# Performance work log

Measured on AMD Instinct MI355X. Metric: run time of the kernel, lower is better.

The kernel has to match this reference:

```python
import jax, jax.numpy as jnp
from jax import lax
import numpy as np


def setup_inputs() -> dict:
    key = jax.random.key(0)
    ks = iter(jax.random.split(key, 48))

    def w(shape):
        fan = shape[0] if len(shape) == 2 else int(np.prod(shape[1:]))
        return jax.random.normal(next(ks), shape, jnp.float32) / np.sqrt(fan)

    def b(n):
        return jax.random.normal(next(ks), (n,), jnp.float32) * 0.01

    T = 16
    return dict(
        search=jax.random.normal(next(ks), (3, 383, 287), jnp.float32),
        exemplars=jax.random.normal(next(ks), (T, 3, 383, 287), jnp.float32),
        # AlexNet features (random-weight stand-in for pretrained)
        aw1=w((64, 3, 11, 11)), ab1=b(64),
        aw2=w((192, 64, 5, 5)), ab2=b(192),
        aw3=w((384, 192, 3, 3)), ab3=b(384),
        aw4=w((256, 384, 3, 3)), ab4=b(256),
        aw5=w((256, 256, 3, 3)), ab5=b(256),
        # conv_deconv: Conv1d(256,256,3,p=1) -> MaxPool1d(88) -> ConvTranspose1d(256,256,88)
        wcd=w((256, 256, 3)), bcd=b(256),
        wt=w((256, 256, 88)), bt=b(256),
        # st_gcn: GCN(256, 512, 256)
        ws1=w((256, 512)), bs1=b(512),
        ws2=w((512, 256)), bs2=b(256),
        # g, h: 1x1 Conv1d(256,256) == linear maps
        wg=w((256, 256)), bg=b(256),
        wh=w((256, 256)), bh=b(256),
        # ct_gcn: GCN(256, 384, 256)
        wc1=w((256, 384)), bc1=b(384),
        wc2=w((384, 256)), bc2=b(256),
    )


def _gct_forward(search, exemplars, aw1, ab1, aw2, ab2, aw3, ab3, aw4, ab4,
                 aw5, ab5, wcd, bcd, wt, bt, ws1, bs1, ws2, bs2,
                 wg, bg, wh, bh, wc1, bc1, wc2, bc2):
    f32 = jnp.float32

    def conv2d(x, w, bias, s, p):
        y = lax.conv_general_dilated(x, w, (s, s), [(p, p), (p, p)],
                                     dimension_numbers=('NCHW', 'OIHW', 'NCHW'))
        return y + bias[None, :, None, None]

    def maxpool(x):  # k=3, s=2, VALID (AlexNet pools)
        return lax.reduce_window(x, -jnp.inf, lax.max, (1, 1, 3, 3), (1, 1, 2, 2), 'VALID')

    def features(x):
        x = maxpool(jax.nn.relu(conv2d(x, aw1, ab1, 4, 2)))
        x = maxpool(jax.nn.relu(conv2d(x, aw2, ab2, 1, 2)))
        x = jax.nn.relu(conv2d(x, aw3, ab3, 1, 1))
        x = jax.nn.relu(conv2d(x, aw4, ab4, 1, 1))
        x = maxpool(jax.nn.relu(conv2d(x, aw5, ab5, 1, 1)))
        return x

    lrelu = lambda v: jax.nn.leaky_relu(v, 0.01)

    X = features(search[None])          # [1,256,11,8]
    Z = features(exemplars)             # [T,256,11,8]
    T = Z.shape[0]
    D = X.shape[1]                      # 256
    M = X.shape[2] * X.shape[3]         # 88
    Xf = X.reshape(D, M)                # [256,88]
    Zf = Z.reshape(T, D, M)             # [T,256,88]

    # conv_deconv branch: conv1d(k=3,p=1) -> global maxpool -> conv_transpose(k=M)
    xc = lax.conv_general_dilated(Xf[None], wcd, (1,), [(1, 1)],
                                  dimension_numbers=('NCH', 'OIH', 'NCH'))[0] + bcd[:, None]
    v = jnp.max(xc, axis=1)                              # [256]
    X_hat = jnp.einsum('i,iok->ok', v, wt) + bt[:, None]  # [256,88]

    # spatiotemporal graph: A[i+T*j, i+T*k]=1 for j!=k; self-loops for t!=0
    TM = T * M
    n = jnp.arange(TM)
    same_t = (n[:, None] % T) == (n[None, :] % T)
    diff_s = (n[:, None] // T) != (n[None, :] // T)
    A1 = (same_t & diff_s).astype(f32) + jnp.diag((n % T != 0).astype(f32))

    # st GCN over TM nodes (node n = t + T*m -> spatial-major flatten)
    nodes = Zf.transpose(2, 0, 1).reshape(TM, D)          # [TM,256]
    h1 = lrelu(A1 @ (nodes @ ws1) + bs1)                  # [TM,512]
    h2 = lrelu(A1 @ (h1 @ ws2) + bs2)                     # [TM,256]
    V1 = jnp.max(h2.reshape(M, T, D), axis=1).T           # temporal max-pool -> [256,88]

    # dynamic cross-track graph: pairwise g/h affinities + row softmax (fused)
    Vx = V1 + X_hat                                       # [256,88]
    G = wg @ Vx + bg[:, None]                             # [256,88]
    Hh = wh @ Vx + bh[:, None]                            # [256,88]
    A2 = jax.nn.softmax(Hh.T @ G, axis=1)                 # [88,88], A2[j,i]=g(i).h(j)

    # ct GCN
    xv = V1.T                                             # [88,256]
    c1 = lrelu(A2 @ (xv @ wc1) + bc1)                     # [88,384]
    V2 = lrelu(A2 @ (c1 @ wc2) + bc2).T                   # [256,88]

    # F.conv2d(X[1,256,11,8], V2[1,256,11,8]) -> full-overlap correlation = scalar
    R = jnp.sum(Xf * V2).reshape(1, 1, 1, 1)
    return R


def reference(search, exemplars, aw1, ab1, aw2, ab2, aw3, ab3, aw4, ab4,
              aw5, ab5, wcd, bcd, wt, bt, ws1, bs1, ws2, bs2,
              wg, bg, wh, bh, wc1, bc1, wc2, bc2):
    return _gct_forward(search, exemplars, aw1, ab1, aw2, ab2, aw3, ab3, aw4, ab4,
                        aw5, ab5, wcd, bcd, wt, bt, ws1, bs1, ws2, bs2,
                        wg, bg, wh, bh, wc1, bc1, wc2, bc2)
```

## Files before the change

### kernel.cpp

```cpp
#include <hip/hip_runtime.h>
#include <hip/hip_bf16.h>
#include <math.h>

#define BATCH 17
#define T_EX 16
#define H0 383
#define W0 287
#define C1 64
#define H1 95
#define W1 71
#define H1P 47
#define W1P 35
#define C2 192
#define H2P 23
#define W2P 17
#define C3 384
#define C45 256
#define H5P 11
#define W5P 8
#define DD 256
#define MM 88
#define TM 1408

#define HP1 389
#define WP1 292

typedef unsigned short ushort_t;
typedef __attribute__((ext_vector_type(8))) short short8;
typedef __attribute__((ext_vector_type(4))) float f32x4;

__device__ __forceinline__ float lrelu(float v) { return v > 0.f ? v : 0.01f * v; }

__device__ __forceinline__ ushort_t f2bf(float f) {
    unsigned int u = __float_as_uint(f);
    unsigned int r = (u + 0x7fffu + ((u >> 16) & 1u)) >> 16;
    return (ushort_t)r;
}
__device__ __forceinline__ float b2f(ushort_t b) {
    return __uint_as_float(((unsigned int)b) << 16);
}
__device__ __forceinline__ short8 ld16(const ushort_t* p) { return *(const short8*)p; }
__device__ __forceinline__ short8 ld2x8(const ushort_t* p) {
    union { uint2 u[2]; short8 s; } uu;
    uu.u[0] = *(const uint2*)p;
    uu.u[1] = *(const uint2*)(p + 4);
    return uu.s;
}
__device__ __forceinline__ void async_cp16(ushort_t* l, const ushort_t* g) {
    __builtin_amdgcn_global_load_lds(
        (const __attribute__((address_space(1))) void*)g,
        (__attribute__((address_space(3))) void*)l, 16, 0, 0);
}

__global__ void zfill_k(float4* __restrict__ p, int n4) {
    int idx = blockIdx.x * 256 + threadIdx.x;
    if (idx < n4) p[idx] = (float4){0.f, 0.f, 0.f, 0.f};
}

__global__ void prep1_k(const float* __restrict__ search, const float* __restrict__ exemp,
                        ushort_t* __restrict__ out) {
    int idx = blockIdx.x * 256 + threadIdx.x;
    if (idx >= BATCH * H0 * W0) return;
    int ix = idx % W0; int t = idx / W0;
    int iy = t % H0; int b = t / H0;
    const float* src = (b == 0) ? search : exemp + (size_t)(b - 1) * 3 * H0 * W0;
    const int hw = H0 * W0;
    float v0 = src[iy * W0 + ix];
    float v1 = src[hw + iy * W0 + ix];
    float v2 = src[2 * hw + iy * W0 + ix];
    ushort4 o;
    o.x = f2bf(v0); o.y = f2bf(v1); o.z = f2bf(v2); o.w = 0;
    *(ushort4*)&out[(((size_t)b * HP1 + iy + 2) * WP1 + ix + 2) * 4] = o;
}

__global__ void wprep_k(const float* __restrict__ w, ushort_t* __restrict__ out,
                        int KH, int KWl, int KWr, int CINl, int CINr,
                        int NKS, int nch) {
    int idx = blockIdx.x * 256 + threadIdx.x;
    if (idx >= nch) return;
    int c = idx & 255;
    int rest = idx >> 8;
    int ks = rest % NKS;
    int ocb = rest / NKS;
    int k8 = c >> 6, m = c & 63;
    int oc = ocb * 64 + m;
    int KWC = KWl * CINl;
    ushort_t* o = out + (size_t)idx * 8;
#pragma unroll
    for (int j = 0; j < 8; ++j) {
        int kg = ks * 32 + k8 * 8 + j;
        int ky = kg / KWC; int rem = kg - ky * KWC;
        int kx = rem / CINl; int ic = rem - kx * CINl;
        float v = 0.f;
        if (ky < KH && kx < KWr && ic < CINr)
            v = w[(((size_t)oc * CINr + ic) * KH + ky) * KWr + kx];
        o[j] = f2bf(v);
    }
}

__global__ void wprep_gemm_k(const float* __restrict__ ws1, const float* __restrict__ ws2,
                             const float* __restrict__ wcd, ushort_t* __restrict__ WS1T,
                             ushort_t* __restrict__ WS2T, ushort_t* __restrict__ WCDT) {
    int idx = blockIdx.x * 256 + threadIdx.x;
    const float* src; ushort_t* dst; int NKS, mode = 0, sa = 1, sk = 0, base;
    if (idx < 16384)       { src = ws1; dst = WS1T; NKS = 8;  sk = 512; base = idx; }
    else if (idx < 32768)  { src = ws2; dst = WS2T; NKS = 16; sk = 256; base = idx - 16384; }
    else if (idx < 57344)  { src = wcd; dst = WCDT; NKS = 24; mode = 1; base = idx - 32768; }
    else return;
    int c = base & 255;
    int rest = base >> 8;
    int ks = rest % NKS;
    int ocb = rest / NKS;
    int k8 = c >> 6, m = c & 63;
    int oc = ocb * 64 + m;
    ushort_t* o = dst + (size_t)base * 8;
#pragma unroll
    for (int j = 0; j < 8; ++j) {
        int kg = ks * 32 + k8 * 8 + j;
        float v;
        if (mode == 0) v = src[(size_t)oc * sa + (size_t)kg * sk];
        else           v = src[(size_t)oc * 768 + (kg & 255) * 3 + (kg >> 8)];
        o[j] = f2bf(v);
    }
}

template <int STRIDE, bool A16>
__global__ __launch_bounds__(256) void conv_mfma5(
    const ushort_t* __restrict__ inp, const ushort_t* __restrict__ wt,
    const float* __restrict__ bias, ushort_t* __restrict__ out,
    int Hp, int Wp, int C, int Wout, int HW, int NKS2, int KWl,
    int OHp, int OWp, int OPAD, int COUT) {
    const int tid = threadIdx.x;
    const int wv = tid >> 6, lane = tid & 63;
    const int quad = lane >> 4, l16 = lane & 15;
    const int n_blk = blockIdx.x * 64;
    const int ocb = blockIdx.y;
    const int b = blockIdx.z;

    __shared__ ushort_t As[2][4096];
    __shared__ ushort_t Bs[2][4096];
    __shared__ int offs[432];

    const int KWC = KWl * C;
    for (int g = tid; g < NKS2 * 8; g += 256) {
        int kg = g * 8;
        int ky = kg / KWC; int rem = kg - ky * KWC;
        int kx = rem / C; int c8 = rem - kx * C;
        offs[g] = (ky * Wp + kx) * C + c8;
    }

    const ushort_t* inb = inp + (size_t)b * Hp * Wp * C;
    int n_g = n_blk + lane;
    int n_gc = n_g < HW ? n_g : HW - 1;
    int oy = n_gc / Wout, ox = n_gc - oy * Wout;
    const int base0 = (oy * STRIDE * Wp + ox * STRIDE) * C;

    f32x4 acc[4];
#pragma unroll
    for (int cn = 0; cn < 4; ++cn) acc[cn] = (f32x4){0.f, 0.f, 0.f, 0.f};

    const ushort_t* wblk = wt + (size_t)ocb * (size_t)NKS2 * 4096;

    __syncthreads();

    {
        const ushort_t* aS = wblk + tid * 8;
        async_cp16(&As[0][tid * 8], aS);
        async_cp16(&As[0][2048 + tid * 8], aS + 2048);
        const int o0 = offs[wv], o1 = offs[4 + wv];
        if (A16) {
            async_cp16(&Bs[0][tid * 8], inb + base0 + o0);
            async_cp16(&Bs[0][2048 + tid * 8], inb + base0 + o1);
        } else {
            *(short8*)&Bs[0][tid * 8] = ld2x8(inb + base0 + o0);
            *(short8*)&Bs[0][2048 + tid * 8] = ld2x8(inb + base0 + o1);
        }
    }
    __syncthreads();

    for (int ks2 = 0; ks2 < NKS2; ++ks2) {
        const int cur = ks2 & 1, nxt = cur ^ 1;
        if (ks2 + 1 < NKS2) {
            const ushort_t* aS = wblk + (size_t)(ks2 + 1) * 4096 + tid * 8;
            async_cp16(&As[nxt][tid * 8], aS);
            async_cp16(&As[nxt][2048 + tid * 8], aS + 2048);
            const int o0 = offs[(ks2 + 1) * 8 + wv], o1 = offs[(ks2 + 1) * 8 + 4 + wv];
            if (A16) {
                async_cp16(&Bs[nxt][tid * 8], inb + base0 + o0);
                async_cp16(&Bs[nxt][2048 + tid * 8], inb + base0 + o1);
            } else {
                *(short8*)&Bs[nxt][tid * 8] = ld2x8(inb + base0 + o0);
                *(short8*)&Bs[nxt][2048 + tid * 8] = ld2x8(inb + base0 + o1);
            }
        }
#pragma unroll
        for (int h = 0; h < 2; ++h) {
            const short8 af = *(const short8*)&As[cur][h * 2048 + (quad * 64 + wv * 16 + l16) * 8];
#pragma unroll
            for (int cn = 0; cn < 4; ++cn) {
                const short8 bfr = *(const short8*)&Bs[cur][h * 2048 + (quad * 64 + cn * 16 + l16) * 8];
                acc[cn] = __builtin_amdgcn_mfma_f32_16x16x32_bf16(af, bfr, acc[cn], 0, 0, 0);
            }
        }
        __syncthreads();
    }

    const int oc0 = ocb * 64 + wv * 16 + quad * 4;
    const float bi0 = bias[oc0], bi1 = bias[oc0 + 1], bi2 = bias[oc0 + 2], bi3 = bias[oc0 + 3];
#pragma unroll
    for (int cn = 0; cn < 4; ++cn) {
        int n = n_blk + cn * 16 + l16;
        if (n < HW) {
            int y = n / Wout, x = n - y * Wout;
            size_t base = (((size_t)b * OHp + y + OPAD) * OWp + x + OPAD) * COUT + oc0;
            ushort4 o;
            o.x = f2bf(fmaxf(acc[cn][0] + bi0, 0.f));
            o.y = f2bf(fmaxf(acc[cn][1] + bi1, 0.f));
            o.z = f2bf(fmaxf(acc[cn][2] + bi2, 0.f));
            o.w = f2bf(fmaxf(acc[cn][3] + bi3, 0.f));
            *(ushort4*)&out[base] = o;
        }
    }
}

template <int MODE, bool HASBIAS, bool SC1>
__global__ __launch_bounds__(256) void gemm_mfma3(
    const ushort_t* __restrict__ Bsrc, const ushort_t* __restrict__ wt,
    const float* __restrict__ bias, float* __restrict__ out,
    int RS, int N, int NKS, int sn, int sc) {
    const int tid = threadIdx.x;
    const int wv = tid >> 6, lane = tid & 63;
    const int quad = lane >> 4, l16 = lane & 15;
    const int n_blk = blockIdx.x * 64;
    const int ocb = blockIdx.y;

    __shared__ ushort_t Bs[2][2048];

    int n_g = n_blk + lane;
    int n_gc = n_g < N ? n_g : N - 1;
    int row = (MODE == 1) ? (1 + (n_gc & 15)) * MM + (n_gc >> 4) : n_gc;
    const size_t base0 = (size_t)row * RS;

    f32x4 acc[4];
#pragma unroll
    for (int cn = 0; cn < 4; ++cn) acc[cn] = (f32x4){0.f, 0.f, 0.f, 0.f};

    const ushort_t* wblk = wt + (size_t)ocb * NKS * 2048;
    const int afrag = (quad * 64 + wv * 16 + l16) * 8;

    short8 a0 = ld16(wblk + afrag);
    *(short8*)&Bs[0][tid * 8] = ld16(Bsrc + base0 + wv * 8);
    __syncthreads();

    for (int ks = 0; ks < NKS; ++ks) {
        const int cur = ks & 1, nxt = cur ^ 1;
        short8 a1, bn;
        const bool more = (ks + 1 < NKS);
        if (more) {
            a1 = ld16(wblk + (ks + 1) * 2048 + afrag);
            bn = ld16(Bsrc + base0 + (ks + 1) * 32 + wv * 8);
        }
#pragma unroll
        for (int cn = 0; cn < 4; ++cn) {
            const short8 bfr = *(const short8*)&Bs[cur][(quad * 64 + cn * 16 + l16) * 8];
            acc[cn] = __builtin_amdgcn_mfma_f32_16x16x32_bf16(a0, bfr, acc[cn], 0, 0, 0);
        }
        if (more) *(short8*)&Bs[nxt][tid * 8] = bn;
        a0 = a1;
        __syncthreads();
    }

    const int oc0 = ocb * 64 + wv * 16 + quad * 4;
    float bb[4] = {0.f, 0.f, 0.f, 0.f};
    if (HASBIAS) { bb[0] = bias[oc0]; bb[1] = bias[oc0+1]; bb[2] = bias[oc0+2]; bb[3] = bias[oc0+3]; }
#pragma unroll
    for (int cn = 0; cn < 4; ++cn) {
        int n = n_blk + cn * 16 + l16;
        if (n < N) {
            if (SC1) {
                float4 o;
                o.x = acc[cn][0] + bb[0]; o.y = acc[cn][1] + bb[1];
                o.z = acc[cn][2] + bb[2]; o.w = acc[cn][3] + bb[3];
                *(float4*)&out[(size_t)n * sn + oc0] = o;
            } else {
#pragma unroll
                for (int reg = 0; reg < 4; ++reg)
                    out[(size_t)n * sn + (size_t)(oc0 + reg) * sc] = acc[cn][reg] + bb[reg];
            }
        }
    }
}

__global__ void pool_nhwc(const ushort_t* __restrict__ in, ushort_t* __restrict__ out,
                          int C, int Hin, int Win, int Hout, int Wout,
                          int OHp, int OWp, int OPAD) {
    int total = BATCH * C * Hout * Wout;
    int idx = blockIdx.x * 256 + threadIdx.x;
    if (idx >= total) return;
    int c = idx % C; int r = idx / C;
    int x = r % Wout; r /= Wout;
    int y = r % Hout; int b = r / Hout;
    const int rs = Win * C;
    const ushort_t* p = in + (((size_t)b * Hin + 2 * y) * Win + 2 * x) * C + c;
    float m = b2f(p[0]);
    m = fmaxf(m, b2f(p[C])); m = fmaxf(m, b2f(p[2 * C]));
    m = fmaxf(m, b2f(p[rs])); m = fmaxf(m, b2f(p[rs + C])); m = fmaxf(m, b2f(p[rs + 2 * C]));
    m = fmaxf(m, b2f(p[2 * rs])); m = fmaxf(m, b2f(p[2 * rs + C])); m = fmaxf(m, b2f(p[2 * rs + 2 * C]));
    out[(((size_t)b * OHp + y + OPAD) * OWp + x + OPAD) * C + c] = f2bf(m);
}

__global__ void pool5_k(const ushort_t* __restrict__ in, float* __restrict__ P,
                        ushort_t* __restrict__ PB, ushort_t* __restrict__ XfPad) {
    int total = BATCH * 256 * MM;
    int idx = blockIdx.x * 256 + threadIdx.x;
    if (idx >= total) return;
    int c = idx % 256; int r = idx / 256;
    int x = r % W5P; r /= W5P;
    int y = r % H5P; int b = r / H5P;
    const int rs = W2P * 256;
    const ushort_t* p = in + (((size_t)b * H2P + 2 * y) * W2P + 2 * x) * 256 + c;
    float m = b2f(p[0]);
    m = fmaxf(m, b2f(p[256])); m = fmaxf(m, b2f(p[512]));
    m = fmaxf(m, b2f(p[rs])); m = fmaxf(m, b2f(p[rs + 256])); m = fmaxf(m, b2f(p[rs + 512]));
    m = fmaxf(m, b2f(p[2 * rs])); m = fmaxf(m, b2f(p[2 * rs + 256])); m = fmaxf(m, b2f(p[2 * rs + 512]));
    int mm = y * W5P + x;
    size_t o = ((size_t)b * MM + mm) * 256 + c;
    P[o] = m;
    ushort_t mb = f2bf(m);
    PB[o] = mb;
    if (b == 0) XfPad[(size_t)(mm + 1) * 256 + c] = mb;
}

__global__ void vmax_k(const float* __restrict__ xc, float* __restrict__ v) {
    int c = blockIdx.x * 64 + threadIdx.x;
    float m = -INFINITY;
    for (int j = 0; j < MM; ++j) m = fmaxf(m, xc[(size_t)c * MM + j]);
    v[c] = m;
}

__global__ void xhat_k(const float* __restrict__ v, const float* __restrict__ wt,
                       const float* __restrict__ bt, float* __restrict__ xhat) {
    __shared__ float lv[256];
    for (int j = threadIdx.x; j < 256; j += 256) lv[j] = v[j];
    __syncthreads();
    int idx = blockIdx.x * 256 + threadIdx.x;
    if (idx >= DD * MM) return;
    int k = idx % MM, o = idx / MM;
    float acc = bt[o];
    for (int i = 0; i < 256; ++i) acc = fmaf(lv[i], wt[(i * 256 + o) * MM + k], acc);
    xhat[idx] = acc;
}

__global__ void s1_k(const float* __restrict__ Y1, float* __restrict__ S1) {
    int idx = blockIdx.x * 256 + threadIdx.x;
    if (idx >= T_EX * 512) return;
    int c = idx % 512, t = idx / 512;
    float acc = 0.f;
    for (int m = 0; m < MM; ++m) acc += Y1[(m * T_EX + t) * 512 + c];
    S1[idx] = acc;
}

__global__ void h1_k(const float* __restrict__ Y1, const float* __restrict__ S1,
                     const float* __restrict__ bs1, ushort_t* __restrict__ h1b) {
    int idx = blockIdx.x * 256 + threadIdx.x;
    if (idx >= TM * 512) return;
    int c = idx % 512; int n = idx / 512;
    int t = n % T_EX;
    float val = S1[t * 512 + c] + bs1[c];
    if (t == 0) val -= Y1[idx];
    h1b[idx] = f2bf(lrelu(val));
}

__global__ void s2_k(const float* __restrict__ Y2, float* __restrict__ S2) {
    int idx = blockIdx.x * 256 + threadIdx.x;
    if (idx >= T_EX * 256) return;
    int c = idx % 256, t = idx / 256;
    float acc = 0.f;
    for (int m = 0; m < MM; ++m) acc += Y2[(m * T_EX + t) * 256 + c];
    S2[idx] = acc;
}

__global__ void h2_k(const float* __restrict__ Y2, const float* __restrict__ S2,
                     const float* __restrict__ bs2, float* __restrict__ h2) {
    int idx = blockIdx.x * 256 + threadIdx.x;
    if (idx >= TM * 256) return;
    int c = idx % 256; int n = idx / 256;
    int t = n % T_EX;
    float val = S2[t * 256 + c] + bs2[c];
    if (t == 0) val -= Y2[idx];
    h2[idx] = lrelu(val);
}

__global__ void v1vx_k(const float* __restrict__ h2, const float* __restrict__ xhat,
                       float* __restrict__ V1, float* __restrict__ Vx) {
    int idx = blockIdx.x * 256 + threadIdx.x;
    if (idx >= DD * MM) return;
    int m = idx % MM, d = idx / MM;
    float mx = -INFINITY;
    for (int t = 0; t < T_EX; ++t) mx = fmaxf(mx, h2[(m * T_EX + t) * 256 + d]);
    V1[idx] = mx;
    Vx[idx] = mx + xhat[idx];
}

__global__ void lin88_k(const float* __restrict__ Wg, const float* __restrict__ bg,
                        const float* __restrict__ Wh, const float* __restrict__ bh,
                        const float* __restrict__ Vin, float* __restrict__ Gout,
                        float* __restrict__ Hout) {
    int idx = blockIdx.x * 256 + threadIdx.x;
    if (idx >= DD * MM) return;
    const float* W = blockIdx.y ? Wh : Wg;
    const float* bias = blockIdx.y ? bh : bg;
    float* out = blockIdx.y ? Hout : Gout;
    int m = idx % MM, o = idx / MM;
    const float* wr = W + o * 256;
    float acc = bias[o];
    for (int i = 0; i < 256; ++i) acc = fmaf(wr[i], Vin[i * MM + m], acc);
    out[idx] = acc;
}

__global__ void smsm_k(const float* __restrict__ Hh, const float* __restrict__ G,
                       float* __restrict__ A2) {
    int j = blockIdx.x;
    int tid = threadIdx.x;
    __shared__ float row[96];
    __shared__ float red[128];
    for (int i = tid; i < MM; i += 128) {
        float acc = 0.f;
        for (int c = 0; c < 256; ++c) acc = fmaf(Hh[c * MM + j], G[c * MM + i], acc);
        row[i] = acc;
    }
    __syncthreads();
    float val = (tid < MM) ? row[tid] : -INFINITY;
    red[tid] = val; __syncthreads();
    for (int s = 64; s > 0; s >>= 1) {
        if (tid < s) red[tid] = fmaxf(red[tid], red[tid + s]);
        __syncthreads();
    }
    float mx = red[0]; __syncthreads();
    float e = (tid < MM) ? expf(val - mx) : 0.f;
    red[tid] = e; __syncthreads();
    for (int s = 64; s > 0; s >>= 1) {
        if (tid < s) red[tid] += red[tid + s];
        __syncthreads();
    }
    float inv = 1.f / red[0];
    if (tid < MM) A2[j * MM + tid] = e * inv;
}

__global__ void t1_k(const float* __restrict__ V1, const float* __restrict__ wc1,
                     float* __restrict__ t1) {
    int idx = blockIdx.x * 256 + threadIdx.x;
    if (idx >= MM * 384) return;
    int c = idx % 384, m = idx / 384;
    float acc = 0.f;
    for (int d = 0; d < 256; ++d) acc = fmaf(V1[d * MM + m], wc1[d * 384 + c], acc);
    t1[idx] = acc;
}

__global__ void c1_k(const float* __restrict__ A2, const float* __restrict__ t1,
                     const float* __restrict__ bc1, float* __restrict__ c1) {
    int idx = blockIdx.x * 256 + threadIdx.x;
    if (idx >= MM * 384) return;
    int c = idx % 384, j = idx / 384;
    float acc = bc1[c];
    for (int i = 0; i < MM; ++i) acc = fmaf(A2[j * MM + i], t1[i * 384 + c], acc);
    c1[idx] = lrelu(acc);
}

__global__ void t2_k(const float* __restrict__ c1, const float* __restrict__ wc2,
                     float* __restrict__ t2) {
    int idx = blockIdx.x * 256 + threadIdx.x;
    if (idx >= MM * 256) return;
    int c = idx % 256, m = idx / 256;
    const float* cr = c1 + m * 384;
    float acc = 0.f;
    for (int d = 0; d < 384; ++d) acc = fmaf(cr[d], wc2[d * 256 + c], acc);
    t2[idx] = acc;
}

__global__ void v2_k(const float* __restrict__ A2, const float* __restrict__ t2,
                     const float* __restrict__ bc2, float* __restrict__ V2m) {
    int idx = blockIdx.x * 256 + threadIdx.x;
    if (idx >= MM * 256) return;
    int c = idx % 256, j = idx / 256;
    float acc = bc2[c];
    for (int i = 0; i < MM; ++i) acc = fmaf(A2[j * MM + i], t2[i * 256 + c], acc);
    V2m[idx] = lrelu(acc);
}

__global__ void final_k(const float* __restrict__ Xf2, const float* __restrict__ V2m,
                        float* __restrict__ out) {
    __shared__ float red[256];
    float acc = 0.f;
    for (int idx = threadIdx.x; idx < DD * MM; idx += 256)
        acc = fmaf(Xf2[idx], V2m[idx], acc);
    red[threadIdx.x] = acc; __syncthreads();
    for (int s = 128; s > 0; s >>= 1) {
        if (threadIdx.x < s) red[threadIdx.x] += red[threadIdx.x + s];
        __syncthreads();
    }
    if (threadIdx.x == 0) out[0] = red[0];
}

extern "C" void kernel_launch(void* const* d_in, const int* in_sizes, int n_in,
                              void* d_out, int out_size, void* d_ws, size_t ws_size,
                              hipStream_t stream) {
    const float* search = (const float*)d_in[0];
    const float* exemp  = (const float*)d_in[1];
    const float* aw1 = (const float*)d_in[2];  const float* ab1 = (const float*)d_in[3];
    const float* aw2 = (const float*)d_in[4];  const float* ab2 = (const float*)d_in[5];
    const float* aw3 = (const float*)d_in[6];  const float* ab3 = (const float*)d_in[7];
    const float* aw4 = (const float*)d_in[8];  const float* ab4 = (const float*)d_in[9];
    const float* aw5 = (const float*)d_in[10]; const float* ab5 = (const float*)d_in[11];
    const float* wcd = (const float*)d_in[12]; const float* bcd = (const float*)d_in[13];
    const float* wt  = (const float*)d_in[14]; const float* bt  = (const float*)d_in[15];
    const float* ws1 = (const float*)d_in[16]; const float* bs1 = (const float*)d_in[17];
    const float* ws2 = (const float*)d_in[18]; const float* bs2 = (const float*)d_in[19];
    const float* wg  = (const float*)d_in[20]; const float* bg  = (const float*)d_in[21];
    const float* wh  = (const float*)d_in[22]; const float* bh  = (const float*)d_in[23];
    const float* wc1 = (const float*)d_in[24]; const float* bc1 = (const float*)d_in[25];
    const float* wc2 = (const float*)d_in[26]; const float* bc2 = (const float*)d_in[27];

    float* ws = (float*)d_ws;
    float* R1 = ws;
    float* R2 = ws + 3870720;
    float* R3 = ws + 7544832;
    float* Wg = ws + 8628864;

    ushort_t* in1p  = (ushort_t*)R1;
    ushort_t* c1out = (ushort_t*)R2;
    ushort_t* p1out = (ushort_t*)R3;
    ushort_t* c2out = (ushort_t*)R1;
    ushort_t* p2out = (ushort_t*)R2;
    ushort_t* c3out = (ushort_t*)(R2 + 775200);
    ushort_t* c4out = (ushort_t*)R1;
    ushort_t* c5out = (ushort_t*)R3;
    ushort_t* WT    = (ushort_t*)Wg;

    zfill_k<<<(965500 + 255) / 256, 256, 0, stream>>>((float4*)R1, 965500);
    prep1_k<<<(BATCH * H0 * W0 + 255) / 256, 256, 0, stream>>>(search, exemp, in1p);
    wprep_k<<<(4608 + 255) / 256, 256, 0, stream>>>(aw1, WT, 11, 12, 11, 4, 3, 18, 4608);
    conv_mfma5<4, false><<<dim3(106, 1, BATCH), 256, 0, stream>>>(
        in1p, WT, ab1, c1out, HP1, WP1, 4, W1, H1 * W1, 9, 12, H1, W1, 0, 64);
    zfill_k<<<(270504 + 255) / 256, 256, 0, stream>>>((float4*)R3, 270504);
    pool_nhwc<<<(BATCH * 64 * H1P * W1P + 255) / 256, 256, 0, stream>>>(
        c1out, p1out, 64, H1, W1, H1P, W1P, 51, 39, 2);
    wprep_k<<<(38400 + 255) / 256, 256, 0, stream>>>(aw2, WT, 5, 5, 5, 64, 64, 50, 38400);
    conv_mfma5<1, true><<<dim3(26, 3, BATCH), 256, 0, stream>>>(
        p1out, WT, ab2, c2out, 51, 39, 64, W1P, H1P * W1P, 25, 5, H1P, W1P, 0, 192);
    zfill_k<<<(581400 + 255) / 256, 256, 0, stream>>>((float4*)R2, 581400);
    pool_nhwc<<<(BATCH * 192 * H2P * W2P + 255) / 256, 256, 0, stream>>>(
        c2out, p2out, 192, H1P, W1P, H2P, W2P, 25, 19, 1);
    wprep_k<<<(82944 + 255) / 256, 256, 0, stream>>>(aw3, WT, 3, 3, 3, 192, 192, 54, 82944);
    conv_mfma5<1, true><<<dim3(7, 6, BATCH), 256, 0, stream>>>(
        p2out, WT, ab3, c3out, 25, 19, 192, W2P, H2P * W2P, 27, 3, 25, 19, 1, 384);
    zfill_k<<<(258400 + 255) / 256, 256, 0, stream>>>((float4*)R1, 258400);
    wprep_k<<<(110592 + 255) / 256, 256, 0, stream>>>(aw4, WT, 3, 3, 3, 384, 384, 108, 110592);
    conv_mfma5<1, true><<<dim3(7, 4, BATCH), 256, 0, stream>>>(
        c3out, WT, ab4, c4out, 25, 19, 384, W2P, H2P * W2P, 54, 3, 25, 19, 1, 256);
    wprep_k<<<(73728 + 255) / 256, 256, 0, stream>>>(aw5, WT, 3, 3, 3, 256, 256, 72, 73728);
    conv_mfma5<1, true><<<dim3(7, 4, BATCH), 256, 0, stream>>>(
        c4out, WT, ab5, c5out, 25, 19, 256, W2P, H2P * W2P, 36, 3, H2P, W2P, 0, 256);

    float*    P      = R1 + 2417664;
    ushort_t* PB     = (ushort_t*)(R1 + 2800640);
    ushort_t* XfPad  = (ushort_t*)(R1 + 2992128);
    float*    xc     = R1 + 3003648;

    ushort_t* WS1T = (ushort_t*)Wg;
    ushort_t* WS2T = (ushort_t*)(Wg + 65536);
    ushort_t* WCDT = (ushort_t*)(Wg + 131072);
    wprep_gemm_k<<<(57344 + 255) / 256, 256, 0, stream>>>(ws1, ws2, wcd, WS1T, WS2T, WCDT);

    pool5_k<<<(BATCH * 256 * MM + 255) / 256, 256, 0, stream>>>(c5out, P, PB, XfPad);
    float* Xf2 = P;

    float* v_   = R1 + 0;
    float* xhat = R1 + 1024;
    float* Y1   = R1 + 23552;
    float* S1   = R1 + 744448;
    ushort_t* h1b = (ushort_t*)(R1 + 752640);
    float* Y2   = R1 + 1473536;
    float* S2   = R1 + 1833984;
    float* h2   = R1 + 1838080;
    float* V1   = R1 + 2198528;
    float* Vx   = R1 + 2221056;
    float* G    = R1 + 2243584;
    float* Hh   = R1 + 2266112;
    float* A2   = R1 + 2296832;
    float* t1   = R1 + 2305024;
    float* c1   = R1 + 2338816;
    float* t2   = R1 + 2372608;
    float* V2m  = R1 + 2395136;

    gemm_mfma3<0, true, false><<<dim3(2, 4), 256, 0, stream>>>(
        XfPad, WCDT, bcd, xc, 256, MM, 24, 1, MM);
    vmax_k<<<4, 64, 0, stream>>>(xc, v_);
    xhat_k<<<(DD * MM + 255) / 256, 256, 0, stream>>>(v_, wt, bt, xhat);

    gemm_mfma3<1, false, true><<<dim3(22, 8), 256, 0, stream>>>(
        PB, WS1T, nullptr, Y1, 256, TM, 8, 512, 1);
    s1_k<<<(T_EX * 512 + 255) / 256, 256, 0, stream>>>(Y1, S1);
    h1_k<<<(TM * 512 + 255) / 256, 256, 0, stream>>>(Y1, S1, bs1, h1b);
    gemm_mfma3<0, false, true><<<dim3(22, 4), 256, 0, stream>>>(
        h1b, WS2T, nullptr, Y2, 512, TM, 16, 256, 1);
    s2_k<<<(T_EX * 256 + 255) / 256, 256, 0, stream>>>(Y2, S2);
    h2_k<<<(TM * 256 + 255) / 256, 256, 0, stream>>>(Y2, S2, bs2, h2);
    v1vx_k<<<(DD * MM + 255) / 256, 256, 0, stream>>>(h2, xhat, V1, Vx);

    lin88_k<<<dim3((DD * MM + 255) / 256, 2), 256, 0, stream>>>(wg, bg, wh, bh, Vx, G, Hh);
    smsm_k<<<MM, 128, 0, stream>>>(Hh, G, A2);

    t1_k<<<(MM * 384 + 255) / 256, 256, 0, stream>>>(V1, wc1, t1);
    c1_k<<<(MM * 384 + 255) / 256, 256, 0, stream>>>(A2, t1, bc1, c1);
    t2_k<<<(MM * 256 + 255) / 256, 256, 0, stream>>>(c1, wc2, t2);
    v2_k<<<(MM * 256 + 255) / 256, 256, 0, stream>>>(A2, t2, bc2, V2m);

    final_k<<<1, 256, 0, stream>>>(Xf2, V2m, (float*)d_out);
}
```

Baseline: 545.5 us.

## Use two-wave conv blocks with 32x64 per-wave tiles for more operand reuse

The implicit-GEMM conv kernel now uses 128 threads (2 waves) per 64x64 output tile, with each wave computing two 16-row MFMA blocks that share the same B fragments. This halves LDS reads of B per MFMA and raises register-level reuse. Staging loops are widened so fewer threads fill the same shared tiles. STRIDE becomes a runtime argument instead of a template parameter, which may cost some address arithmetic and reduce latency hiding per block because fewer waves are resident.

```diff
diff --git a/kernel.cpp b/kernel.cpp
--- a/kernel.cpp
+++ b/kernel.cpp
@@ -124,11 +124,11 @@
     }
 }
 
-template <int STRIDE, bool A16>
-__global__ __launch_bounds__(256) void conv_mfma5(
+template <bool A16>
+__global__ __launch_bounds__(128) void conv_mfma7(
     const ushort_t* __restrict__ inp, const ushort_t* __restrict__ wt,
     const float* __restrict__ bias, ushort_t* __restrict__ out,
-    int Hp, int Wp, int C, int Wout, int HW, int NKS2, int KWl,
+    int Hp, int Wp, int C, int Wout, int HW, int NKS2, int KWl, int STRIDE,
     int OHp, int OWp, int OPAD, int COUT) {
     const int tid = threadIdx.x;
     const int wv = tid >> 6, lane = tid & 63;
@@ -142,7 +142,7 @@
     __shared__ int offs[432];
 
     const int KWC = KWl * C;
-    for (int g = tid; g < NKS2 * 8; g += 256) {
+    for (int g = tid; g < NKS2 * 8; g += 128) {
         int kg = g * 8;
         int ky = kg / KWC; int rem = kg - ky * KWC;
         int kx = rem / C; int c8 = rem - kx * C;
@@ -150,75 +150,89 @@
     }
 
     const ushort_t* inb = inp + (size_t)b * Hp * Wp * C;
-    int n_g = n_blk + lane;
+    int n_g = n_blk + (tid & 63);
     int n_gc = n_g < HW ? n_g : HW - 1;
     int oy = n_gc / Wout, ox = n_gc - oy * Wout;
     const int base0 = (oy * STRIDE * Wp + ox * STRIDE) * C;
 
-    f32x4 acc[4];
-#pragma unroll
-    for (int cn = 0; cn < 4; ++cn) acc[cn] = (f32x4){0.f, 0.f, 0.f, 0.f};
+    f32x4 acc[2][4];
+#pragma unroll
+    for (int rm = 0; rm < 2; ++rm)
+#pragma unroll
+        for (int cn = 0; cn < 4; ++cn) acc[rm][cn] = (f32x4){0.f, 0.f, 0.f, 0.f};
 
     const ushort_t* wblk = wt + (size_t)ocb * (size_t)NKS2 * 4096;
 
     __syncthreads();
 
-    {
-        const ushort_t* aS = wblk + tid * 8;
-        async_cp16(&As[0][tid * 8], aS);
-        async_cp16(&As[0][2048 + tid * 8], aS + 2048);
-        const int o0 = offs[wv], o1 = offs[4 + wv];
-        if (A16) {
-            async_cp16(&Bs[0][tid * 8], inb + base0 + o0);
-            async_cp16(&Bs[0][2048 + tid * 8], inb + base0 + o1);
-        } else {
-            *(short8*)&Bs[0][tid * 8] = ld2x8(inb + base0 + o0);
-            *(short8*)&Bs[0][2048 + tid * 8] = ld2x8(inb + base0 + o1);
-        }
-    }
+#define STAGE_A(buf, ks2v)                                                   \
+    {                                                                        \
+        const ushort_t* tb = wblk + (size_t)(ks2v) * 4096;                   \
+        _Pragma("unroll")                                                    \
+        for (int p = 0; p < 4; ++p) {                                        \
+            int idx = p * 128 + tid;                                         \
+            async_cp16(&As[buf][idx * 8], tb + idx * 8);                     \
+        }                                                                    \
+    }
+#define STAGE_B(buf, ks2v)                                                   \
+    {                                                                        \
+        _Pragma("unroll")                                                    \
+        for (int p = 0; p < 4; ++p) {                                        \
+            int idx = p * 128 + tid;                \
+            int hh = idx >> 8, k8 = (idx >> 6) & 3;                          \
+            const ushort_t* s = inb + base0 + offs[(ks2v) * 8 + hh * 4 + k8];\
+            if (A16) async_cp16(&Bs[buf][idx * 8], s);                       \
+            else     *(short8*)&Bs[buf][idx * 8] = ld2x8(s);                 \
+        }                                                                    \
+    }
+
+    STAGE_A(0, 0)
+    STAGE_B(0, 0)
     __syncthreads();
 
     for (int ks2 = 0; ks2 < NKS2; ++ks2) {
         const int cur = ks2 & 1, nxt = cur ^ 1;
         if (ks2 + 1 < NKS2) {
-            const ushort_t* aS = wblk + (size_t)(ks2 + 1) * 4096 + tid * 8;
-            async_cp16(&As[nxt][tid * 8], aS);
-            async_cp16(&As[nxt][2048 + tid * 8], aS + 2048);
-            const int o0 = offs[(ks2 + 1) * 8 + wv], o1 = offs[(ks2 + 1) * 8 + 4 + wv];
-            if (A16) {
-                async_cp16(&Bs[nxt][tid * 8], inb + base0 + o0);
-                async_cp16(&Bs[nxt][2048 + tid * 8], inb + base0 + o1);
-            } else {
-                *(short8*)&Bs[nxt][tid * 8] = ld2x8(inb + base0 + o0);
-                *(short8*)&Bs[nxt][2048 + tid * 8] = ld2x8(inb + base0 + o1);
-            }
+            STAGE_A(nxt, ks2 + 1)
+            STAGE_B(nxt, ks2 + 1)
         }
 #pragma unroll
         for (int h = 0; h < 2; ++h) {
-            const short8 af = *(const short8*)&As[cur][h * 2048 + (quad * 64 + wv * 16 + l16) * 8];
+            const int abase = h * 256 + quad * 64;
+            const short8 a0 = *(const short8*)&As[cur][(abase + wv * 32 + l16) * 8];
+            const short8 a1 = *(const short8*)&As[cur][(abase + wv * 32 + 16 + l16) * 8];
+            short8 bf[4];
+#pragma unroll
+            for (int cn = 0; cn < 4; ++cn)
+                bf[cn] = *(const short8*)&Bs[cur][(abase + cn * 16 + l16) * 8];
 #pragma unroll
             for (int cn = 0; cn < 4; ++cn) {
-                const short8 bfr = *(const short8*)&Bs[cur][h * 2048 + (quad * 64 + cn * 16 + l16) * 8];
-                acc[cn] = __builtin_amdgcn_mfma_f32_16x16x32_bf16(af, bfr, acc[cn], 0, 0, 0);
+                acc[0][cn] = __builtin_amdgcn_mfma_f32_16x16x32_bf16(a0, bf[cn], acc[0][cn], 0, 0, 0);
+                acc[1][cn] = __builtin_amdgcn_mfma_f32_16x16x32_bf16(a1, bf[cn], acc[1][cn], 0, 0, 0);
             }
         }
         __syncthreads();
     }
-
-    const int oc0 = ocb * 64 + wv * 16 + quad * 4;
-    const float bi0 = bias[oc0], bi1 = bias[oc0 + 1], bi2 = bias[oc0 + 2], bi3 = bias[oc0 + 3];
-#pragma unroll
-    for (int cn = 0; cn < 4; ++cn) {
-        int n = n_blk + cn * 16 + l16;
-        if (n < HW) {
-            int y = n / Wout, x = n - y * Wout;
-            size_t base = (((size_t)b * OHp + y + OPAD) * OWp + x + OPAD) * COUT + oc0;
-            ushort4 o;
-            o.x = f2bf(fmaxf(acc[cn][0] + bi0, 0.f));
-            o.y = f2bf(fmaxf(acc[cn][1] + bi1, 0.f));
-            o.z = f2bf(fmaxf(acc[cn][2] + bi2, 0.f));
-            o.w = f2bf(fmaxf(acc[cn][3] + bi3, 0.f));
-            *(ushort4*)&out[base] = o;
+#undef STAGE_A
+#undef STAGE_B
+
+#pragma unroll
+    for (int rm = 0; rm < 2; ++rm) {
+        const int ocr = ocb * 64 + wv * 32 + rm * 16 + quad * 4;
+        const float bi0 = bias[ocr], bi1 = bias[ocr + 1], bi2 = bias[ocr + 2], bi3 = bias[ocr + 3];
+#pragma unroll
+        for (int cn = 0; cn < 4; ++cn) {
+            int n = n_blk + cn * 16 + l16;
+            if (n < HW) {
+                int y = n / Wout, x = n - y * Wout;
+                size_t base = (((size_t)b * OHp + y + OPAD) * OWp + x + OPAD) * COUT + ocr;
+                ushort4 o;
+                o.x = f2bf(fmaxf(acc[rm][cn][0] + bi0, 0.f));
+                o.y = f2bf(fmaxf(acc[rm][cn][1] + bi1, 0.f));
+                o.z = f2bf(fmaxf(acc[rm][cn][2] + bi2, 0.f));
+                o.w = f2bf(fmaxf(acc[rm][cn][3] + bi3, 0.f));
+                *(ushort4*)&out[base] = o;
+            }
         }
     }
 }
@@ -540,27 +554,27 @@
     zfill_k<<<(965500 + 255) / 256, 256, 0, stream>>>((float4*)R1, 965500);
     prep1_k<<<(BATCH * H0 * W0 + 255) / 256, 256, 0, stream>>>(search, exemp, in1p);
     wprep_k<<<(4608 + 255) / 256, 256, 0, stream>>>(aw1, WT, 11, 12, 11, 4, 3, 18, 4608);
-    conv_mfma5<4, false><<<dim3(106, 1, BATCH), 256, 0, stream>>>(
-        in1p, WT, ab1, c1out, HP1, WP1, 4, W1, H1 * W1, 9, 12, H1, W1, 0, 64);
+    conv_mfma7<false><<<dim3(106, 1, BATCH), 128, 0, stream>>>(
+        in1p, WT, ab1, c1out, HP1, WP1, 4, W1, H1 * W1, 9, 12, 4, H1, W1, 0, 64);
     zfill_k<<<(270504 + 255) / 256, 256, 0, stream>>>((float4*)R3, 270504);
     pool_nhwc<<<(BATCH * 64 * H1P * W1P + 255) / 256, 256, 0, stream>>>(
         c1out, p1out, 64, H1, W1, H1P, W1P, 51, 39, 2);
     wprep_k<<<(38400 + 255) / 256, 256, 0, stream>>>(aw2, WT, 5, 5, 5, 64, 64, 50, 38400);
-    conv_mfma5<1, true><<<dim3(26, 3, BATCH), 256, 0, stream>>>(
-        p1out, WT, ab2, c2out, 51, 39, 64, W1P, H1P * W1P, 25, 5, H1P, W1P, 0, 192);
+    conv_mfma7<true><<<dim3(26, 3, BATCH), 128, 0, stream>>>(
+        p1out, WT, ab2, c2out, 51, 39, 64, W1P, H1P * W1P, 25, 5, 1, H1P, W1P, 0, 192);
     zfill_k<<<(581400 + 255) / 256, 256, 0, stream>>>((float4*)R2, 581400);
     pool_nhwc<<<(BATCH * 192 * H2P * W2P + 255) / 256, 256, 0, stream>>>(
         c2out, p2out, 192, H1P, W1P, H2P, W2P, 25, 19, 1);
     wprep_k<<<(82944 + 255) / 256, 256, 0, stream>>>(aw3, WT, 3, 3, 3, 192, 192, 54, 82944);
-    conv_mfma5<1, true><<<dim3(7, 6, BATCH), 256, 0, stream>>>(
-        p2out, WT, ab3, c3out, 25, 19, 192, W2P, H2P * W2P, 27, 3, 25, 19, 1, 384);
+    conv_mfma7<true><<<dim3(7, 6, BATCH), 128, 0, stream>>>(
+        p2out, WT, ab3, c3out, 25, 19, 192, W2P, H2P * W2P, 27, 3, 1, 25, 19, 1, 384);
     zfill_k<<<(258400 + 255) / 256, 256, 0, stream>>>((float4*)R1, 258400);
     wprep_k<<<(110592 + 255) / 256, 256, 0, stream>>>(aw4, WT, 3, 3, 3, 384, 384, 108, 110592);
-    conv_mfma5<1, true><<<dim3(7, 4, BATCH), 256, 0, stream>>>(
-        c3out, WT, ab4, c4out, 25, 19, 384, W2P, H2P * W2P, 54, 3, 25, 19, 1, 256);
+    conv_mfma7<true><<<dim3(7, 4, BATCH), 128, 0, stream>>>(
+        c3out, WT, ab4, c4out, 25, 19, 384, W2P, H2P * W2P, 54, 3, 1, 25, 19, 1, 256);
     wprep_k<<<(73728 + 255) / 256, 256, 0, stream>>>(aw5, WT, 3, 3, 3, 256, 256, 72, 73728);
-    conv_mfma5<1, true><<<dim3(7, 4, BATCH), 256, 0, stream>>>(
-        c4out, WT, ab5, c5out, 25, 19, 256, W2P, H2P * W2P, 36, 3, H2P, W2P, 0, 256);
+    conv_mfma7<true><<<dim3(7, 4, BATCH), 128, 0, stream>>>(
+        c4out, WT, ab5, c5out, 25, 19, 256, W2P, H2P * W2P, 36, 3, 1, H2P, W2P, 0, 256);
 
     float*    P      = R1 + 2417664;
     ushort_t* PB     = (ushort_t*)(R1 + 2800640);
```

After: 583.4 us. 1.07x slower.
